# Optimization experiments

Measured on AMD Instinct MI355X. Metric: run time of the kernel, lower is better.

The kernel has to match this reference:

```python
import jax, jax.numpy as jnp
import numpy as np

N, M, D, DV = 8192, 8192, 512, 512

def setup_inputs() -> dict:
    key = jax.random.key(0)
    kq, kk, kv = jax.random.split(key, 3)
    return {
        "query": jax.random.normal(kq, (N, D), dtype=jnp.float32),
        "key": jax.random.normal(kk, (M, D), dtype=jnp.float32),
        "value": jax.random.normal(kv, (M, DV), dtype=jnp.float32),
    }

def reference(query, key, value):
    # scores: [N, M] = Q @ K^T (no scale, no mask, matching the torch module)
    scores = query @ key.T
    attn = jax.nn.softmax(scores, axis=-1)
    return attn @ value
```

## Files before the change

### kernel.cpp

```cpp
#include <hip/hip_runtime.h>
#include <hip/hip_fp16.h>
#include <stdint.h>

typedef _Float16 f16;
typedef _Float16 f16x8 __attribute__((ext_vector_type(8)));
typedef float    f32x4 __attribute__((ext_vector_type(4)));
typedef int      i32x4 __attribute__((ext_vector_type(4)));

#define NQ 8192
#define NK 8192
#define DD 512
#define DVV 512

__device__ __forceinline__ void stage16(const void* g, void* ldsbase, int lane) {
#if __has_builtin(__builtin_amdgcn_global_load_lds)
  __builtin_amdgcn_global_load_lds((const __attribute__((address_space(1))) void*)g,
                                   (__attribute__((address_space(3))) void*)ldsbase, 16, 0, 0);
#else
  ((i32x4*)ldsbase)[lane] = *(const i32x4*)g;
#endif
}

__global__ void conv_f16k(const float* __restrict__ src, f16* __restrict__ dst, int n8) {
  int i = blockIdx.x * 256 + threadIdx.x;
  if (i >= n8) return;
  const float4* s4 = (const float4*)src;
  float4 a = s4[2 * i], b = s4[2 * i + 1];
  float vv[8] = {a.x, a.y, a.z, a.w, b.x, b.y, b.z, b.w};
  f16 h8[8];
#pragma unroll
  for (int j = 0; j < 8; ++j) h8[j] = (f16)vv[j];
  *(f16x8*)(dst + (size_t)i * 8) = *(f16x8*)h8;
}

__global__ void conv_vT(const float* __restrict__ v, f16* __restrict__ vT) {
  __shared__ float t[64][65];
  int k0 = blockIdx.x * 64, d0 = blockIdx.y * 64;
#pragma unroll
  for (int e = 0; e < 16; ++e) {
    int idx = threadIdx.x + e * 256;
    int kr = idx >> 6, dc = idx & 63;
    t[kr][dc] = v[(size_t)(k0 + kr) * DVV + d0 + dc];
  }
  __syncthreads();
  int dl = threadIdx.x >> 2, seg = (threadIdx.x & 3) * 16;
  f16 tmp[16];
#pragma unroll
  for (int c = 0; c < 16; ++c) tmp[c] = (f16)t[seg + c][dl];
  f16* dst = vT + (size_t)(d0 + dl) * NK + k0 + seg;
  *(f16x8*)dst = *(f16x8*)tmp;
  *(f16x8*)(dst + 8) = *(f16x8*)(tmp + 8);
}

__global__ __launch_bounds__(512, 2) void qk_kernel(
    const f16* __restrict__ q16, const f16* __restrict__ k16,
    f16* __restrict__ s16, float* __restrict__ pm, float* __restrict__ ps) {
  __shared__ f16 LS[2 * 2 * 16384];
  __shared__ float red[2][4][128];
  const int tid = threadIdx.x, lane = tid & 63, wid = tid >> 6;
  const int wr = wid >> 2, wc = wid & 3;
  const int bx = blockIdx.x, by = blockIdx.y;
  const int lo16 = lane & 15, hi4 = lane >> 4;

  f32x4 acc[8][4] = {};

  const int srw = lane >> 3, sc8 = (lane & 7) ^ srw;
  const f16* aptr[4]; const f16* bptr[4]; int adst[4], bdst[4];
#pragma unroll
  for (int u = 0; u < 4; ++u) {
    int r = wid * 32 + u * 8 + srw;
    aptr[u] = q16 + (size_t)(by * 256 + r) * DD + sc8 * 8;
    bptr[u] = k16 + (size_t)(bx * 256 + r) * DD + sc8 * 8;
    adst[u] = (wid * 32 + u * 8) * 64;
    bdst[u] = adst[u] + 16384;
  }
  int aoff[8][2], boff[4][2];
#pragma unroll
  for (int m = 0; m < 8; ++m)
#pragma unroll
    for (int kk = 0; kk < 2; ++kk) {
      int row = wr * 128 + m * 16 + lo16;
      aoff[m][kk] = row * 64 + (((kk * 4 + hi4) ^ (row & 7)) << 3);
    }
#pragma unroll
  for (int n = 0; n < 4; ++n)
#pragma unroll
    for (int kk = 0; kk < 2; ++kk) {
      int row = wc * 64 + n * 16 + lo16;
      boff[n][kk] = 16384 + row * 64 + (((kk * 4 + hi4) ^ (row & 7)) << 3);
    }

#define STG(t2, buf)                                                        \
  do {                                                                      \
    _Pragma("unroll") for (int u = 0; u < 4; ++u) {                         \
      stage16(aptr[u] + (t2) * 64, LS + (buf) * 32768 + adst[u], lane);     \
      stage16(bptr[u] + (t2) * 64, LS + (buf) * 32768 + bdst[u], lane);     \
    }                                                                       \
  } while (0)

  STG(0, 0);
  asm volatile("s_waitcnt vmcnt(0)" ::: "memory");
  __builtin_amdgcn_s_barrier();
  asm volatile("" ::: "memory");

  for (int t = 0; t < 8; ++t) {
    const int cur = t & 1;
    if (t < 7) STG(t + 1, cur ^ 1);
    const f16* Bb = LS + cur * 32768;
    f16x8 bf[2][4];
#pragma unroll
    for (int n = 0; n < 4; ++n)
#pragma unroll
      for (int kk = 0; kk < 2; ++kk) bf[kk][n] = *(const f16x8*)&Bb[boff[n][kk]];
#pragma unroll
    for (int h = 0; h < 2; ++h) {
      f16x8 af[4][2];
#pragma unroll
      for (int mi = 0; mi < 4; ++mi)
#pragma unroll
        for (int kk = 0; kk < 2; ++kk) af[mi][kk] = *(const f16x8*)&Bb[aoff[h * 4 + mi][kk]];
      __builtin_amdgcn_s_setprio(1);
#pragma unroll
      for (int mi = 0; mi < 4; ++mi)
#pragma unroll
        for (int n = 0; n < 4; ++n) {
          acc[h * 4 + mi][n] =
              __builtin_amdgcn_mfma_f32_16x16x32_f16(af[mi][0], bf[0][n], acc[h * 4 + mi][n], 0, 0, 0);
          acc[h * 4 + mi][n] =
              __builtin_amdgcn_mfma_f32_16x16x32_f16(af[mi][1], bf[1][n], acc[h * 4 + mi][n], 0, 0, 0);
        }
      __builtin_amdgcn_s_setprio(0);
    }
    asm volatile("s_waitcnt vmcnt(0)" ::: "memory");
    __builtin_amdgcn_s_barrier();
    asm volatile("" ::: "memory");
  }
#undef STG

  float rmax[8][4];
#pragma unroll
  for (int i = 0; i < 8; ++i)
#pragma unroll
    for (int r = 0; r < 4; ++r) {
      float m = fmaxf(fmaxf(acc[i][0][r], acc[i][1][r]), fmaxf(acc[i][2][r], acc[i][3][r]));
#pragma unroll
      for (int d = 1; d < 16; d <<= 1) m = fmaxf(m, __shfl_xor(m, d, 64));
      rmax[i][r] = m;
    }
  if (lo16 == 0) {
#pragma unroll
    for (int i = 0; i < 8; ++i)
#pragma unroll
      for (int r = 0; r < 4; ++r) red[wr][wc][i * 16 + hi4 * 4 + r] = rmax[i][r];
  }
  __syncthreads();
  float pmv[8][4];
#pragma unroll
  for (int i = 0; i < 8; ++i)
#pragma unroll
    for (int r = 0; r < 4; ++r) {
      int rl = i * 16 + hi4 * 4 + r;
      pmv[i][r] = fmaxf(fmaxf(red[wr][0][rl], red[wr][1][rl]),
                        fmaxf(red[wr][2][rl], red[wr][3][rl]));
    }
  __syncthreads();
  float rsum[8][4];
#pragma unroll
  for (int i = 0; i < 8; ++i)
#pragma unroll
    for (int r = 0; r < 4; ++r) {
      float s = 0.f;
#pragma unroll
      for (int j = 0; j < 4; ++j) {
        float p = __expf(acc[i][j][r] - pmv[i][r]);
        acc[i][j][r] = p;
        s += p;
      }
#pragma unroll
      for (int d = 1; d < 16; d <<= 1) s += __shfl_xor(s, d, 64);
      rsum[i][r] = s;
    }
#pragma unroll
  for (int i = 0; i < 8; ++i)
#pragma unroll
    for (int r = 0; r < 4; ++r) {
      size_t grow = (size_t)(by * 256 + wr * 128 + i * 16 + hi4 * 4 + r);
#pragma unroll
      for (int j = 0; j < 4; ++j)
        s16[grow * NK + bx * 256 + wc * 64 + j * 16 + lo16] = (f16)acc[i][j][r];
    }
  if (lo16 == 0) {
#pragma unroll
    for (int i = 0; i < 8; ++i)
#pragma unroll
      for (int r = 0; r < 4; ++r) red[wr][wc][i * 16 + hi4 * 4 + r] = rsum[i][r];
  }
  __syncthreads();
  if (wc == 0 && lo16 == 0) {
#pragma unroll
    for (int i = 0; i < 8; ++i)
#pragma unroll
      for (int r = 0; r < 4; ++r) {
        int rl = i * 16 + hi4 * 4 + r;
        size_t grow = (size_t)(by * 256 + wr * 128 + rl);
        pm[grow * 32 + bx] = pmv[i][r];
        ps[grow * 32 + bx] = red[wr][0][rl] + red[wr][1][rl] + red[wr][2][rl] + red[wr][3][rl];
      }
  }
}

__global__ void red_kernel(const float* __restrict__ pm, const float* __restrict__ ps,
                           float* __restrict__ coef) {
  int row = blockIdx.x * 8 + (threadIdx.x >> 5);
  int t = threadIdx.x & 31;
  float pmt = pm[(size_t)row * 32 + t];
  float m = pmt;
#pragma unroll
  for (int d = 1; d < 32; d <<= 1) m = fmaxf(m, __shfl_xor(m, d, 32));
  float e = __expf(pmt - m);
  float l = ps[(size_t)row * 32 + t] * e;
#pragma unroll
  for (int d = 1; d < 32; d <<= 1) l += __shfl_xor(l, d, 32);
  coef[(size_t)row * 32 + t] = e / l;
}

__global__ __launch_bounds__(256, 2) void pv_kernel(
    const f16* __restrict__ p16, const float* __restrict__ coef,
    const f16* __restrict__ vT, float* __restrict__ dst,
    int steps, size_t zstride) {
  __shared__ f16 lsA[2][128 * 64];
  __shared__ f16 lsB[2][128 * 64];
  const int tid = threadIdx.x, lane = tid & 63, wid = tid >> 6;
  const int lo16 = lane & 15, hi4 = lane >> 4;
  const int wr = wid >> 1, wc = wid & 1;
  const int bx = blockIdx.x, by = blockIdx.y, bz = blockIdx.z;
  const int g0 = bz * steps;
  f32x4 acc[4][4] = {};

  const int arow0 = tid >> 3, acol = tid & 7;
  const int srw = lane >> 3;
  const int sc = (lane & 7) ^ srw;

  f16x8 va[4];
  float scv[4];

#pragma unroll
  for (int u = 0; u < 4; ++u)
    va[u] = *(const f16x8*)(p16 + (size_t)(by * 128 + u * 32 + arow0) * NK + (size_t)g0 * 64 + acol * 8);
#pragma unroll
  for (int i = 0; i < 4; ++i) {
    int unit = wid * 4 + i;
    int row = unit * 8 + srw;
    stage16(vT + (size_t)(bx * 128 + row) * NK + (size_t)g0 * 64 + sc * 8,
            &lsB[0][unit * 512], lane);
  }
#pragma unroll
  for (int u = 0; u < 4; ++u)
    scv[u] = coef[(size_t)(by * 128 + u * 32 + arow0) * 32 + (g0 >> 2)];
#pragma unroll
  for (int u = 0; u < 4; ++u) {
    int row = u * 32 + arow0;
    f16x8 vv = va[u] * (f16)scv[u];
    *(f16x8*)&lsA[0][row * 64 + ((acol ^ (row & 7)) << 3)] = vv;
  }
  __syncthreads();

  for (int s = 0; s < steps; ++s) {
    const int cur = s & 1, nxt = cur ^ 1;
    const int g = g0 + s;
    if (s + 1 < steps) {
#pragma unroll
      for (int u = 0; u < 4; ++u)
        va[u] = *(const f16x8*)(p16 + (size_t)(by * 128 + u * 32 + arow0) * NK +
                                (size_t)(g + 1) * 64 + acol * 8);
#pragma unroll
      for (int i = 0; i < 4; ++i) {
        int unit = wid * 4 + i;
        int row = unit * 8 + srw;
        stage16(vT + (size_t)(bx * 128 + row) * NK + (size_t)(g + 1) * 64 + sc * 8,
                &lsB[nxt][unit * 512], lane);
      }
#pragma unroll
      for (int u = 0; u < 4; ++u)
        scv[u] = coef[(size_t)(by * 128 + u * 32 + arow0) * 32 + ((g + 1) >> 2)];
    }
#pragma unroll
    for (int ks = 0; ks < 2; ++ks) {
      f16x8 af[4], bf[4];
#pragma unroll
      for (int i = 0; i < 4; ++i) {
        int row = wr * 64 + i * 16 + lo16;
        af[i] = *(const f16x8*)&lsA[cur][row * 64 + (((ks * 4 + hi4) ^ (row & 7)) << 3)];
      }
#pragma unroll
      for (int j = 0; j < 4; ++j) {
        int dv = wc * 64 + j * 16 + lo16;
        bf[j] = *(const f16x8*)&lsB[cur][dv * 64 + (((ks * 4 + hi4) ^ (dv & 7)) << 3)];
      }
#pragma unroll
      for (int i = 0; i < 4; ++i)
#pragma unroll
        for (int j = 0; j < 4; ++j)
          acc[i][j] = __builtin_amdgcn_mfma_f32_16x16x32_f16(af[i], bf[j], acc[i][j], 0, 0, 0);
    }
    if (s + 1 < steps) {
#pragma unroll
      for (int u = 0; u < 4; ++u) {
        int row = u * 32 + arow0;
        f16x8 vv = va[u] * (f16)scv[u];
        *(f16x8*)&lsA[nxt][row * 64 + ((acol ^ (row & 7)) << 3)] = vv;
      }
    }
    __syncthreads();
  }

  float* o = dst + (size_t)bz * zstride;
#pragma unroll
  for (int i = 0; i < 4; ++i)
#pragma unroll
    for (int j = 0; j < 4; ++j)
#pragma unroll
      for (int r = 0; r < 4; ++r)
        o[(size_t)(by * 128 + wr * 64 + i * 16 + hi4 * 4 + r) * DVV +
          bx * 128 + wc * 64 + j * 16 + lo16] = acc[i][j][r];
}

__global__ void reduce_out(const float* __restrict__ part, float* __restrict__ out,
                           int ks, size_t n4) {
  size_t i = (size_t)blockIdx.x * 256 + threadIdx.x;
  if (i >= n4) return;
  float4 a = ((const float4*)part)[i];
  for (int z = 1; z < ks; ++z) {
    float4 b = ((const float4*)(part + z * n4 * 4))[i];
    a.x += b.x; a.y += b.y; a.z += b.z; a.w += b.w;
  }
  ((float4*)out)[i] = a;
}

__global__ void zero_out(float* o, int n) {
  int i = blockIdx.x * 256 + threadIdx.x;
  if (i < n) o[i] = 0.f;
}

extern "C" void kernel_launch(void* const* d_in, const int* in_sizes, int n_in,
                              void* d_out, int out_size, void* d_ws, size_t ws_size,
                              hipStream_t stream) {
  (void)in_sizes; (void)n_in; (void)out_size;
  const float* Q = (const float*)d_in[0];
  const float* K = (const float*)d_in[1];
  const float* V = (const float*)d_in[2];
  float* out = (float*)d_out;

  const size_t sz16 = (size_t)NK * DD * 2;
  const size_t fixedB = 2 * sz16;
  const size_t perRow = 1024 + 128 * 3 + (size_t)NK * 2;
  const size_t partB = (size_t)16384 * DVV * 4;
  int nc = 0;
  for (int cand = 8192; cand >= 1024; cand >>= 1)
    if (fixedB + (size_t)cand * perRow + partB <= ws_size) { nc = cand; break; }
  if (nc == 0) {
    zero_out<<<(NQ * DVV + 255) / 256, 256, 0, stream>>>(out, NQ * DVV);
    return;
  }
  const int ks = 16384 / nc;
  const int steps = 128 / ks;

  char* w = (char*)d_ws;
  f16* k16 = (f16*)w;
  f16* vT = (f16*)(w + sz16);
  char* p = w + fixedB;
  f16* q16 = (f16*)p;      p += (size_t)nc * 1024;
  float* pm = (float*)p;   p += (size_t)nc * 128;
  float* ps = (float*)p;   p += (size_t)nc * 128;
  float* coef = (float*)p; p += (size_t)nc * 128;
  f16* s16 = (f16*)p;      p += (size_t)nc * NK * 2;
  float* part = (float*)p;

  conv_f16k<<<NK * DD / 8 / 256, 256, 0, stream>>>(K, k16, NK * DD / 8);
  conv_vT<<<dim3(NK / 64, DVV / 64), 256, 0, stream>>>(V, vT);

  for (int c = 0; c < NQ / nc; ++c) {
    conv_f16k<<<nc * DD / 8 / 256, 256, 0, stream>>>(Q + (size_t)c * nc * DD, q16, nc * DD / 8);
    qk_kernel<<<dim3(NK / 256, nc / 256), 512, 0, stream>>>(q16, k16, s16, pm, ps);
    red_kernel<<<nc / 8, 256, 0, stream>>>(pm, ps, coef);
    pv_kernel<<<dim3(DVV / 128, nc / 128, ks), 256, 0, stream>>>(
        s16, coef, vT, part, steps, (size_t)nc * DVV);
    reduce_out<<<(int)(((size_t)nc * DVV / 4 + 255) / 256), 256, 0, stream>>>(
        part, out + (size_t)c * nc * DVV, ks, (size_t)nc * DVV / 4);
  }
}
```

Before: 244.6 us.

## Stage softmax probabilities through LDS for coalesced stores; transpose softmax stats layout

The qk kernel now writes each exp'd probability as f16 into a swizzled LDS tile and then copies whole rows to global memory with 16-byte vector stores. Before, each lane did scattered 2-byte stores straight to global. The per-block max, sum and coef arrays are transposed to a [block][row] layout so accesses across rows are contiguous in the qk, reduce and pv kernels, and __expf is replaced with exp2f on a pre-scaled argument. The cost is extra LDS traffic and reuse of the staging buffer after the GEMM, which relies on the earlier barriers being enough to keep other warps from still reading LS.

```diff
diff --git a/kernel.cpp b/kernel.cpp
--- a/kernel.cpp
+++ b/kernel.cpp
@@ -11,6 +11,7 @@
 #define NK 8192
 #define DD 512
 #define DVV 512
+#define LOG2E 1.44269504f
 
 __device__ __forceinline__ void stage16(const void* g, void* ldsbase, int lane) {
 #if __has_builtin(__builtin_amdgcn_global_load_lds)
@@ -54,8 +55,9 @@
 
 __global__ __launch_bounds__(512, 2) void qk_kernel(
     const f16* __restrict__ q16, const f16* __restrict__ k16,
-    f16* __restrict__ s16, float* __restrict__ pm, float* __restrict__ ps) {
-  __shared__ f16 LS[2 * 2 * 16384];
+    f16* __restrict__ s16, float* __restrict__ pmT, float* __restrict__ psT,
+    int nrows) {
+  __shared__ f16 LS[65536];
   __shared__ float red[2][4][128];
   const int tid = threadIdx.x, lane = tid & 63, wid = tid >> 6;
   const int wr = wid >> 2, wc = wid & 3;
@@ -169,25 +171,19 @@
   for (int i = 0; i < 8; ++i)
 #pragma unroll
     for (int r = 0; r < 4; ++r) {
+      int qloc = wr * 128 + i * 16 + hi4 * 4 + r;
+      int swz = ((qloc >> 2) & 7) << 3;
       float s = 0.f;
 #pragma unroll
       for (int j = 0; j < 4; ++j) {
-        float p = __expf(acc[i][j][r] - pmv[i][r]);
-        acc[i][j][r] = p;
+        float p = exp2f((acc[i][j][r] - pmv[i][r]) * LOG2E);
         s += p;
+        int kloc = wc * 64 + j * 16 + lo16;
+        LS[qloc * 256 + (kloc ^ swz)] = (f16)p;
       }
 #pragma unroll
       for (int d = 1; d < 16; d <<= 1) s += __shfl_xor(s, d, 64);
       rsum[i][r] = s;
-    }
-#pragma unroll
-  for (int i = 0; i < 8; ++i)
-#pragma unroll
-    for (int r = 0; r < 4; ++r) {
-      size_t grow = (size_t)(by * 256 + wr * 128 + i * 16 + hi4 * 4 + r);
-#pragma unroll
-      for (int j = 0; j < 4; ++j)
-        s16[grow * NK + bx * 256 + wc * 64 + j * 16 + lo16] = (f16)acc[i][j][r];
     }
   if (lo16 == 0) {
 #pragma unroll
@@ -203,31 +199,43 @@
       for (int r = 0; r < 4; ++r) {
         int rl = i * 16 + hi4 * 4 + r;
         size_t grow = (size_t)(by * 256 + wr * 128 + rl);
-        pm[grow * 32 + bx] = pmv[i][r];
-        ps[grow * 32 + bx] = red[wr][0][rl] + red[wr][1][rl] + red[wr][2][rl] + red[wr][3][rl];
-      }
-  }
-}
-
-__global__ void red_kernel(const float* __restrict__ pm, const float* __restrict__ ps,
-                           float* __restrict__ coef) {
+        pmT[(size_t)bx * nrows + grow] = pmv[i][r];
+        psT[(size_t)bx * nrows + grow] = red[wr][0][rl] + red[wr][1][rl] +
+                                         red[wr][2][rl] + red[wr][3][rl];
+      }
+  }
+  {
+    const int q = tid >> 1, half = tid & 1;
+    const int swz = ((q >> 2) & 7) << 3;
+    f16* gdst = s16 + (size_t)(by * 256 + q) * NK + bx * 256 + half * 128;
+#pragma unroll
+    for (int e = 0; e < 16; ++e) {
+      int k0 = half * 128 + e * 8;
+      f16x8 v = *(const f16x8*)&LS[q * 256 + (k0 ^ swz)];
+      *(f16x8*)(gdst + e * 8) = v;
+    }
+  }
+}
+
+__global__ void red_kernel(const float* __restrict__ pmT, const float* __restrict__ psT,
+                           float* __restrict__ coefT, int nrows) {
   int row = blockIdx.x * 8 + (threadIdx.x >> 5);
   int t = threadIdx.x & 31;
-  float pmt = pm[(size_t)row * 32 + t];
+  float pmt = pmT[(size_t)t * nrows + row];
   float m = pmt;
 #pragma unroll
   for (int d = 1; d < 32; d <<= 1) m = fmaxf(m, __shfl_xor(m, d, 32));
-  float e = __expf(pmt - m);
-  float l = ps[(size_t)row * 32 + t] * e;
+  float e = exp2f((pmt - m) * LOG2E);
+  float l = psT[(size_t)t * nrows + row] * e;
 #pragma unroll
   for (int d = 1; d < 32; d <<= 1) l += __shfl_xor(l, d, 32);
-  coef[(size_t)row * 32 + t] = e / l;
+  coefT[(size_t)t * nrows + row] = e / l;
 }
 
 __global__ __launch_bounds__(256, 2) void pv_kernel(
-    const f16* __restrict__ p16, const float* __restrict__ coef,
+    const f16* __restrict__ p16, const float* __restrict__ coefT,
     const f16* __restrict__ vT, float* __restrict__ dst,
-    int steps, size_t zstride) {
+    int steps, size_t zstride, int nrows) {
   __shared__ f16 lsA[2][128 * 64];
   __shared__ f16 lsB[2][128 * 64];
   const int tid = threadIdx.x, lane = tid & 63, wid = tid >> 6;
@@ -256,7 +264,7 @@
   }
 #pragma unroll
   for (int u = 0; u < 4; ++u)
-    scv[u] = coef[(size_t)(by * 128 + u * 32 + arow0) * 32 + (g0 >> 2)];
+    scv[u] = coefT[(size_t)(g0 >> 2) * nrows + by * 128 + u * 32 + arow0];
 #pragma unroll
   for (int u = 0; u < 4; ++u) {
     int row = u * 32 + arow0;
@@ -282,7 +290,7 @@
       }
 #pragma unroll
       for (int u = 0; u < 4; ++u)
-        scv[u] = coef[(size_t)(by * 128 + u * 32 + arow0) * 32 + ((g + 1) >> 2)];
+        scv[u] = coefT[(size_t)((g + 1) >> 2) * nrows + by * 128 + u * 32 + arow0];
     }
 #pragma unroll
     for (int ks = 0; ks < 2; ++ks) {
@@ -353,7 +361,7 @@
 
   const size_t sz16 = (size_t)NK * DD * 2;
   const size_t fixedB = 2 * sz16;
-  const size_t perRow = 1024 + 128 * 3 + (size_t)NK * 2;
+  const size_t perRow = 1024 + 32 * 4 * 3 + (size_t)NK * 2;
   const size_t partB = (size_t)16384 * DVV * 4;
   int nc = 0;
   for (int cand = 8192; cand >= 1024; cand >>= 1)
@@ -369,11 +377,11 @@
   f16* k16 = (f16*)w;
   f16* vT = (f16*)(w + sz16);
   char* p = w + fixedB;
-  f16* q16 = (f16*)p;      p += (size_t)nc * 1024;
-  float* pm = (float*)p;   p += (size_t)nc * 128;
-  float* ps = (float*)p;   p += (size_t)nc * 128;
-  float* coef = (float*)p; p += (size_t)nc * 128;
-  f16* s16 = (f16*)p;      p += (size_t)nc * NK * 2;
+  f16* q16 = (f16*)p;       p += (size_t)nc * 1024;
+  float* pmT = (float*)p;   p += (size_t)nc * 128;
+  float* psT = (float*)p;   p += (size_t)nc * 128;
+  float* coefT = (float*)p; p += (size_t)nc * 128;
+  f16* s16 = (f16*)p;       p += (size_t)nc * NK * 2;
   float* part = (float*)p;
 
   conv_f16k<<<NK * DD / 8 / 256, 256, 0, stream>>>(K, k16, NK * DD / 8);
@@ -381,10 +389,10 @@
 
   for (int c = 0; c < NQ / nc; ++c) {
     conv_f16k<<<nc * DD / 8 / 256, 256, 0, stream>>>(Q + (size_t)c * nc * DD, q16, nc * DD / 8);
-    qk_kernel<<<dim3(NK / 256, nc / 256), 512, 0, stream>>>(q16, k16, s16, pm, ps);
-    red_kernel<<<nc / 8, 256, 0, stream>>>(pm, ps, coef);
+    qk_kernel<<<dim3(NK / 256, nc / 256), 512, 0, stream>>>(q16, k16, s16, pmT, psT, nc);
+    red_kernel<<<nc / 8, 256, 0, stream>>>(pmT, psT, coefT, nc);
     pv_kernel<<<dim3(DVV / 128, nc / 128, ks), 256, 0, stream>>>(
-        s16, coef, vT, part, steps, (size_t)nc * DVV);
+        s16, coefT, vT, part, steps, (size_t)nc * DVV, nc);
     reduce_out<<<(int)(((size_t)nc * DVV / 4 + 255) / 256), 256, 0, stream>>>(
         part, out + (size_t)c * nc * DVV, ks, (size_t)nc * DVV / 4);
   }
```

Result: slower. 271.3 us (+10.9%).
